# Kernel tuning notes

Measured on AMD Instinct MI355X. Metric: run time of the kernel, lower is better.

Reference implementation:

```python
import jax, jax.numpy as jnp
import numpy as np


def setup_inputs() -> dict:
    key = jax.random.key(0)
    ks = jax.random.split(key, 7)
    B, C, N, F = 4, 8, 2048, 64
    H, O = 64, 64
    s_in = 1.0 / np.sqrt(F)
    s_h = 1.0 / np.sqrt(H)
    return {
        "x": jax.random.normal(ks[0], (B, C, N, F), dtype=jnp.float32),
        "W1": jax.random.uniform(ks[1], (H, F), jnp.float32, -s_in, s_in),
        "b1": jax.random.uniform(ks[2], (H,), jnp.float32, -s_in, s_in),
        "W2": jax.random.uniform(ks[3], (H, F), jnp.float32, -s_in, s_in),
        "b2": jax.random.uniform(ks[4], (H,), jnp.float32, -s_in, s_in),
        "W3": jax.random.uniform(ks[5], (O, F), jnp.float32, -s_in, s_in),
        "b3": jax.random.uniform(ks[6], (O,), jnp.float32, -s_in, s_in),
    }


def reference(x, W1, b1, W2, b2, W3, b3):
    # e1, e2: [B,C,N,H]  (torch Linear: x @ W^T + b)
    e1 = jnp.einsum("bcnf,hf->bcnh", x, W1) + b1
    e2 = jnp.einsum("bcnf,hf->bcnh", x, W2) + b2
    # adjacency via ReLU(e1 @ e2^T): [B,C,N,N]
    adj = jax.nn.relu(jnp.einsum("bcnh,bcmh->bcnm", e1, e2))
    # propagate: [B,C,N,F]
    h = jnp.einsum("bcnm,bcmf->bcnf", adj, x)
    # output projection (linear3): [B,C,N,O]
    return jnp.einsum("bcnf,of->bcno", h, W3) + b3
```

## Files before the change

### kernel.cpp

```cpp
#include <hip/hip_runtime.h>
#include <hip/hip_bf16.h>

#define BCH 32
#define NN  2048
#define DD  64

typedef __attribute__((ext_vector_type(8)))  __bf16 bf16x8;
typedef __attribute__((ext_vector_type(4)))  __bf16 bf16x4;
typedef __attribute__((ext_vector_type(4)))  float  f32x4;
typedef __attribute__((ext_vector_type(16))) float  f32x16;
typedef __attribute__((ext_vector_type(2)))  int    i32x2;
typedef __attribute__((ext_vector_type(4)))  int    i32x4;
typedef __attribute__((ext_vector_type(2)))  unsigned int u32x2;

__device__ inline f32x4 mfma16(bf16x8 a, bf16x8 b, f32x4 c) {
    return __builtin_amdgcn_mfma_f32_16x16x32_bf16(a, b, c, 0, 0, 0);
}
__device__ inline f32x16 mfma32(bf16x8 a, bf16x8 b, f32x16 c) {
    return __builtin_amdgcn_mfma_f32_32x32x16_bf16(a, b, c, 0, 0, 0);
}
__device__ inline void gload16(const void* g, void* l) {
    __builtin_amdgcn_global_load_lds(
        (const __attribute__((address_space(1))) void*)g,
        (__attribute__((address_space(3))) void*)l, 16, 0, 0);
}
__device__ inline void plswap(int& a, int& b) {
    u32x2 r = __builtin_amdgcn_permlane32_swap((unsigned)a, (unsigned)b, false, false);
    a = (int)r[0];
    b = (int)r[1];
}

__global__ __launch_bounds__(256) void prep_kernel(
    const float* __restrict__ x,
    const float* __restrict__ W1, const float* __restrict__ b1,
    const float* __restrict__ W2, const float* __restrict__ b2,
    const float* __restrict__ W3,
    __bf16* __restrict__ e1f, __bf16* __restrict__ e2f, __bf16* __restrict__ vtf)
{
    const int t   = threadIdx.x;
    const int blk = blockIdx.x;
    const int bc  = blk >> 5, st = blk & 31;
    const long grow = (long)bc * NN + st * 64;
    const int w = t >> 6, l = t & 63, lg = l >> 4, li = l & 15;

    bf16x8 a[4][2];
    #pragma unroll
    for (int nb = 0; nb < 4; ++nb)
        #pragma unroll
        for (int kk = 0; kk < 2; ++kk) {
            const float* p = x + (grow + nb * 16 + li) * DD + kk * 32 + lg * 8;
            f32x4 v0 = *(const f32x4*)p, v1 = *(const f32x4*)(p + 4);
            #pragma unroll
            for (int j = 0; j < 4; ++j) {
                a[nb][kk][j]     = (__bf16)v0[j];
                a[nb][kk][4 + j] = (__bf16)v1[j];
            }
        }

    bf16x8 wf1[2], wf2[2], wf3[2];
    #pragma unroll
    for (int kk = 0; kk < 2; ++kk) {
        const float* p1 = W1 + (w * 16 + li) * DD + kk * 32 + lg * 8;
        const float* p2 = W2 + (w * 16 + li) * DD + kk * 32 + lg * 8;
        const float* p3 = W3 + (w * 16 + li) * DD + kk * 32 + lg * 8;
        f32x4 u0 = *(const f32x4*)p1, u1 = *(const f32x4*)(p1 + 4);
        f32x4 v0 = *(const f32x4*)p2, v1 = *(const f32x4*)(p2 + 4);
        f32x4 t0 = *(const f32x4*)p3, t1 = *(const f32x4*)(p3 + 4);
        #pragma unroll
        for (int j = 0; j < 4; ++j) {
            wf1[kk][j] = (__bf16)u0[j]; wf1[kk][4 + j] = (__bf16)u1[j];
            wf2[kk][j] = (__bf16)v0[j]; wf2[kk][4 + j] = (__bf16)v1[j];
            wf3[kk][j] = (__bf16)t0[j]; wf3[kk][4 + j] = (__bf16)t1[j];
        }
    }
    const f32x4 bq1 = *(const f32x4*)(b1 + w * 16 + lg * 4);
    const f32x4 bq2 = *(const f32x4*)(b2 + w * 16 + lg * 4);

    const size_t tbase = (size_t)(bc * 32 + st) * 4096;

    #pragma unroll
    for (int nb = 0; nb < 4; ++nb) {
        f32x4 acc1 = {0.f,0.f,0.f,0.f}, acc2 = {0.f,0.f,0.f,0.f}, acc3 = {0.f,0.f,0.f,0.f};
        #pragma unroll
        for (int kk = 0; kk < 2; ++kk) {
            acc1 = mfma16(wf1[kk], a[nb][kk], acc1);
            acc2 = mfma16(wf2[kk], a[nb][kk], acc2);
            acc3 = mfma16(a[nb][kk], wf3[kk], acc3);
        }
        bf16x4 q1, q2, q3;
        #pragma unroll
        for (int r = 0; r < 4; ++r) {
            q1[r] = (__bf16)(acc1[r] + bq1[r]);
            q2[r] = (__bf16)(acc2[r] + bq2[r]);
            q3[r] = (__bf16)acc3[r];
        }
        *(bf16x4*)&e1f[tbase + (w * 2 + (lg >> 1)) * 512 + (nb * 16 + li) * 8 + (lg & 1) * 4] = q1;
        *(bf16x4*)&e2f[tbase + (w * 2 + (lg >> 1)) * 512 + (nb * 16 + li) * 8 + (lg & 1) * 4] = q2;
        *(bf16x4*)&vtf[tbase + (nb * 2 + (lg >> 1)) * 512 + (w * 16 + li) * 8 + (lg & 1) * 4] = q3;
    }
}

__global__ __launch_bounds__(512, 1) void fused_kernel(
    const __bf16* __restrict__ e1f, const __bf16* __restrict__ e2f,
    const __bf16* __restrict__ vtf, const float* __restrict__ b3,
    float* __restrict__ out)
{
    __shared__ __align__(16) __bf16 tile[2][8192];

    const int t   = threadIdx.x;
    const int bid = blockIdx.x;
    const int j5  = bid & 31;
    const int bc  = (j5 & 7) * 4 + (j5 >> 3);
    const int nt  = bid >> 5;

    const int w = t >> 6, l = t & 63;
    const int wn = w & 3, wm = w >> 2;
    const int l31 = l & 31, hi5 = l >> 5;
    const int nbase = nt * 256 + wn * 64;

    const float bv0 = b3[l31], bv1 = b3[32 + l31];

    bf16x8 e1v[2][4];
    #pragma unroll
    for (int nb = 0; nb < 2; ++nb) {
        const __bf16* p = e1f + ((size_t)bc * 32 + nt * 4 + wn) * 4096 + hi5 * 512 + (nb * 32 + l31) * 8;
        #pragma unroll
        for (int kk = 0; kk < 4; ++kk)
            e1v[nb][kk] = *(const bf16x8*)(p + kk * 1024);
    }

    f32x16 fz;
    #pragma unroll
    for (int i = 0; i < 16; ++i) fz[i] = 0.f;
    f32x16 hacc[2][2];
    #pragma unroll
    for (int nb = 0; nb < 2; ++nb)
        #pragma unroll
        for (int fb = 0; fb < 2; ++fb)
            #pragma unroll
            for (int i = 0; i < 16; ++i) hacc[nb][fb][i] = 0.f;

    const __bf16* E2T = e2f + (size_t)bc * 131072;
    const __bf16* VTT = vtf + (size_t)bc * 131072;

    auto stage = [&](int buf, int kt) {
        gload16(E2T + (size_t)kt * 4096 + t * 8, &tile[buf][w * 512]);
        gload16(VTT + (size_t)kt * 4096 + t * 8, &tile[buf][4096 + w * 512]);
    };

    stage(0, 0);

    for (int kt = 0; kt < 32; ++kt) {
        const int buf = kt & 1;
        if (kt + 1 < 32) {
            stage(buf ^ 1, kt + 1);
            asm volatile("s_waitcnt vmcnt(2)" ::: "memory");
        } else {
            asm volatile("s_waitcnt vmcnt(0)" ::: "memory");
        }
        __builtin_amdgcn_sched_barrier(0);
        __builtin_amdgcn_s_barrier();

        bf16x8 ef[4];
        #pragma unroll
        for (int kk = 0; kk < 4; ++kk)
            ef[kk] = *(const bf16x8*)&tile[buf][kk * 1024 + hi5 * 512 + (wm * 32 + l31) * 8];

        f32x16 sT[2];
        __builtin_amdgcn_s_setprio(1);
        sT[0] = mfma32(ef[0], e1v[0][0], fz);
        sT[1] = mfma32(ef[0], e1v[1][0], fz);
        #pragma unroll
        for (int kk = 1; kk < 4; ++kk) {
            sT[0] = mfma32(ef[kk], e1v[0][kk], sT[0]);
            sT[1] = mfma32(ef[kk], e1v[1][kk], sT[1]);
        }
        __builtin_amdgcn_s_setprio(0);

        i32x2 Q[2][4];
        #pragma unroll
        for (int nb = 0; nb < 2; ++nb)
            #pragma unroll
            for (int g = 0; g < 4; ++g) {
                bf16x4 q0;
                #pragma unroll
                for (int r = 0; r < 4; ++r)
                    q0[r] = (__bf16)fmaxf(sT[nb][4 * g + r], 0.f);
                Q[nb][g] = __builtin_bit_cast(i32x2, q0);
            }

        bf16x8 vf[4];
        #pragma unroll
        for (int kk2 = 0; kk2 < 2; ++kk2) {
            vf[kk2 * 2 + 0] = *(const bf16x8*)&tile[buf][4096 + (wm * 4 + hi5) * 512 + kk2 * 1024 + l31 * 8];
            vf[kk2 * 2 + 1] = *(const bf16x8*)&tile[buf][4096 + (wm * 4 + hi5) * 512 + kk2 * 1024 + 256 + l31 * 8];
        }
        __builtin_amdgcn_s_setprio(1);
        #pragma unroll
        for (int kk2 = 0; kk2 < 2; ++kk2)
            #pragma unroll
            for (int nb = 0; nb < 2; ++nb) {
                int a0 = Q[nb][2 * kk2][0],     a1 = Q[nb][2 * kk2][1];
                int b0 = Q[nb][2 * kk2 + 1][0], b1 = Q[nb][2 * kk2 + 1][1];
                plswap(a0, b0);
                plswap(a1, b1);
                i32x4 pfi = { a0, a1, b0, b1 };
                bf16x8 pf = __builtin_bit_cast(bf16x8, pfi);
                hacc[nb][0] = mfma32(pf, vf[kk2 * 2 + 0], hacc[nb][0]);
                hacc[nb][1] = mfma32(pf, vf[kk2 * 2 + 1], hacc[nb][1]);
            }
        __builtin_amdgcn_s_setprio(0);

        __builtin_amdgcn_s_barrier();
    }

    float* scratch = (float*)&tile[0][0];
    #pragma unroll
    for (int r2 = 0; r2 < 2; ++r2) {
        __syncthreads();
        if ((wn >> 1) == r2 && wm == 1) {
            #pragma unroll
            for (int nb = 0; nb < 2; ++nb)
                #pragma unroll
                for (int q = 0; q < 8; ++q) {
                    f32x4 v;
                    #pragma unroll
                    for (int r = 0; r < 4; ++r) {
                        const int idx = q * 4 + r;
                        v[r] = hacc[nb][idx >> 4][idx & 15];
                    }
                    *(f32x4*)&scratch[(wn & 1) * 4096 + nb * 2048 + q * 256 + l * 4] = v;
                }
        }
        __syncthreads();
        if ((wn >> 1) == r2 && wm == 0) {
            #pragma unroll
            for (int nb = 0; nb < 2; ++nb)
                #pragma unroll
                for (int q = 0; q < 8; ++q) {
                    f32x4 v = *(const f32x4*)&scratch[(wn & 1) * 4096 + nb * 2048 + q * 256 + l * 4];
                    #pragma unroll
                    for (int r = 0; r < 4; ++r) {
                        const int idx = q * 4 + r;
                        hacc[nb][idx >> 4][idx & 15] += v[r];
                    }
                }
            #pragma unroll
            for (int nb = 0; nb < 2; ++nb) {
                const size_t ob = ((size_t)bc * NN + nbase + nb * 32) * DD;
                #pragma unroll
                for (int reg = 0; reg < 16; ++reg) {
                    const int n = (reg & 3) + 8 * (reg >> 2) + 4 * hi5;
                    out[ob + (size_t)n * DD + l31]      = hacc[nb][0][reg] + bv0;
                    out[ob + (size_t)n * DD + 32 + l31] = hacc[nb][1][reg] + bv1;
                }
            }
        }
    }
}

extern "C" void kernel_launch(void* const* d_in, const int* in_sizes, int n_in,
                              void* d_out, int out_size, void* d_ws, size_t ws_size,
                              hipStream_t stream) {
    const float* x  = (const float*)d_in[0];
    const float* W1 = (const float*)d_in[1];
    const float* b1 = (const float*)d_in[2];
    const float* W2 = (const float*)d_in[3];
    const float* b2 = (const float*)d_in[4];
    const float* W3 = (const float*)d_in[5];
    const float* b3 = (const float*)d_in[6];
    float* out = (float*)d_out;

    __bf16* e1f = (__bf16*)d_ws;
    __bf16* e2f = e1f + (size_t)BCH * NN * DD;
    __bf16* vtf = e2f + (size_t)BCH * NN * DD;

    prep_kernel<<<dim3(1024), dim3(256), 0, stream>>>(x, W1, b1, W2, b2, W3, e1f, e2f, vtf);
    fused_kernel<<<dim3(256), dim3(512), 0, stream>>>(e1f, e2f, vtf, b3, out);
}
```

Measured before the change: 59.56 us.

## Fuse projection prep into attention kernel via cooperative grid sync

Merges the separate projection kernel into the main kernel, launched cooperatively with 256 blocks, and uses a grid-wide sync between the projection phase and the adjacency/propagation phase. Each block computes e1 for its own rows directly into shared memory instead of writing it to global memory and reading it back. e2 and the transformed V still go through global memory. The change removes one kernel launch and the e1 global round-trip. In exchange it adds the cost of a grid barrier, redundant W loads per wave, and extra LDS use that may limit occupancy.

```diff
diff --git a/kernel.cpp b/kernel.cpp
--- a/kernel.cpp
+++ b/kernel.cpp
@@ -1,9 +1,12 @@
 #include <hip/hip_runtime.h>
 #include <hip/hip_bf16.h>
+#include <hip/hip_cooperative_groups.h>
 
 #define BCH 32
 #define NN  2048
 #define DD  64
+
+namespace cg = cooperative_groups;
 
 typedef __attribute__((ext_vector_type(8)))  __bf16 bf16x8;
 typedef __attribute__((ext_vector_type(4)))  __bf16 bf16x4;
@@ -30,82 +33,16 @@
     b = (int)r[1];
 }
 
-__global__ __launch_bounds__(256) void prep_kernel(
+__global__ __launch_bounds__(512, 1) void gcn_kernel(
     const float* __restrict__ x,
     const float* __restrict__ W1, const float* __restrict__ b1,
     const float* __restrict__ W2, const float* __restrict__ b2,
-    const float* __restrict__ W3,
-    __bf16* __restrict__ e1f, __bf16* __restrict__ e2f, __bf16* __restrict__ vtf)
-{
-    const int t   = threadIdx.x;
-    const int blk = blockIdx.x;
-    const int bc  = blk >> 5, st = blk & 31;
-    const long grow = (long)bc * NN + st * 64;
-    const int w = t >> 6, l = t & 63, lg = l >> 4, li = l & 15;
-
-    bf16x8 a[4][2];
-    #pragma unroll
-    for (int nb = 0; nb < 4; ++nb)
-        #pragma unroll
-        for (int kk = 0; kk < 2; ++kk) {
-            const float* p = x + (grow + nb * 16 + li) * DD + kk * 32 + lg * 8;
-            f32x4 v0 = *(const f32x4*)p, v1 = *(const f32x4*)(p + 4);
-            #pragma unroll
-            for (int j = 0; j < 4; ++j) {
-                a[nb][kk][j]     = (__bf16)v0[j];
-                a[nb][kk][4 + j] = (__bf16)v1[j];
-            }
-        }
-
-    bf16x8 wf1[2], wf2[2], wf3[2];
-    #pragma unroll
-    for (int kk = 0; kk < 2; ++kk) {
-        const float* p1 = W1 + (w * 16 + li) * DD + kk * 32 + lg * 8;
-        const float* p2 = W2 + (w * 16 + li) * DD + kk * 32 + lg * 8;
-        const float* p3 = W3 + (w * 16 + li) * DD + kk * 32 + lg * 8;
-        f32x4 u0 = *(const f32x4*)p1, u1 = *(const f32x4*)(p1 + 4);
-        f32x4 v0 = *(const f32x4*)p2, v1 = *(const f32x4*)(p2 + 4);
-        f32x4 t0 = *(const f32x4*)p3, t1 = *(const f32x4*)(p3 + 4);
-        #pragma unroll
-        for (int j = 0; j < 4; ++j) {
-            wf1[kk][j] = (__bf16)u0[j]; wf1[kk][4 + j] = (__bf16)u1[j];
-            wf2[kk][j] = (__bf16)v0[j]; wf2[kk][4 + j] = (__bf16)v1[j];
-            wf3[kk][j] = (__bf16)t0[j]; wf3[kk][4 + j] = (__bf16)t1[j];
-        }
-    }
-    const f32x4 bq1 = *(const f32x4*)(b1 + w * 16 + lg * 4);
-    const f32x4 bq2 = *(const f32x4*)(b2 + w * 16 + lg * 4);
-
-    const size_t tbase = (size_t)(bc * 32 + st) * 4096;
-
-    #pragma unroll
-    for (int nb = 0; nb < 4; ++nb) {
-        f32x4 acc1 = {0.f,0.f,0.f,0.f}, acc2 = {0.f,0.f,0.f,0.f}, acc3 = {0.f,0.f,0.f,0.f};
-        #pragma unroll
-        for (int kk = 0; kk < 2; ++kk) {
-            acc1 = mfma16(wf1[kk], a[nb][kk], acc1);
-            acc2 = mfma16(wf2[kk], a[nb][kk], acc2);
-            acc3 = mfma16(a[nb][kk], wf3[kk], acc3);
-        }
-        bf16x4 q1, q2, q3;
-        #pragma unroll
-        for (int r = 0; r < 4; ++r) {
-            q1[r] = (__bf16)(acc1[r] + bq1[r]);
-            q2[r] = (__bf16)(acc2[r] + bq2[r]);
-            q3[r] = (__bf16)acc3[r];
-        }
-        *(bf16x4*)&e1f[tbase + (w * 2 + (lg >> 1)) * 512 + (nb * 16 + li) * 8 + (lg & 1) * 4] = q1;
-        *(bf16x4*)&e2f[tbase + (w * 2 + (lg >> 1)) * 512 + (nb * 16 + li) * 8 + (lg & 1) * 4] = q2;
-        *(bf16x4*)&vtf[tbase + (nb * 2 + (lg >> 1)) * 512 + (w * 16 + li) * 8 + (lg & 1) * 4] = q3;
-    }
-}
-
-__global__ __launch_bounds__(512, 1) void fused_kernel(
-    const __bf16* __restrict__ e1f, const __bf16* __restrict__ e2f,
-    const __bf16* __restrict__ vtf, const float* __restrict__ b3,
+    const float* __restrict__ W3, const float* __restrict__ b3,
+    __bf16* __restrict__ e2f, __bf16* __restrict__ vtf,
     float* __restrict__ out)
 {
     __shared__ __align__(16) __bf16 tile[2][8192];
+    __shared__ __align__(16) __bf16 e1L[8 * 2048];
 
     const int t   = threadIdx.x;
     const int bid = blockIdx.x;
@@ -114,6 +51,73 @@
     const int nt  = bid >> 5;
 
     const int w = t >> 6, l = t & 63;
+    const int lg = l >> 4, li = l & 15;
+
+    {
+        const long growA = (long)bc * NN + nt * 256 + w * 32;
+
+        bf16x8 a[2][2];
+        #pragma unroll
+        for (int nb = 0; nb < 2; ++nb)
+            #pragma unroll
+            for (int kk = 0; kk < 2; ++kk) {
+                const float* p = x + (growA + nb * 16 + li) * DD + kk * 32 + lg * 8;
+                f32x4 v0 = *(const f32x4*)p, v1 = *(const f32x4*)(p + 4);
+                #pragma unroll
+                for (int j = 0; j < 4; ++j) {
+                    a[nb][kk][j]     = (__bf16)v0[j];
+                    a[nb][kk][4 + j] = (__bf16)v1[j];
+                }
+            }
+
+        const size_t tbase = (size_t)(bc * 32 + nt * 4 + (w >> 1)) * 4096;
+
+        #pragma unroll
+        for (int hb = 0; hb < 4; ++hb) {
+            bf16x8 wf1[2], wf2[2], wf3[2];
+            #pragma unroll
+            for (int kk = 0; kk < 2; ++kk) {
+                const float* p1 = W1 + (hb * 16 + li) * DD + kk * 32 + lg * 8;
+                const float* p2 = W2 + (hb * 16 + li) * DD + kk * 32 + lg * 8;
+                const float* p3 = W3 + (hb * 16 + li) * DD + kk * 32 + lg * 8;
+                f32x4 u0 = *(const f32x4*)p1, u1 = *(const f32x4*)(p1 + 4);
+                f32x4 v0 = *(const f32x4*)p2, v1 = *(const f32x4*)(p2 + 4);
+                f32x4 t0 = *(const f32x4*)p3, t1 = *(const f32x4*)(p3 + 4);
+                #pragma unroll
+                for (int j = 0; j < 4; ++j) {
+                    wf1[kk][j] = (__bf16)u0[j]; wf1[kk][4 + j] = (__bf16)u1[j];
+                    wf2[kk][j] = (__bf16)v0[j]; wf2[kk][4 + j] = (__bf16)v1[j];
+                    wf3[kk][j] = (__bf16)t0[j]; wf3[kk][4 + j] = (__bf16)t1[j];
+                }
+            }
+            const f32x4 bq1 = *(const f32x4*)(b1 + hb * 16 + lg * 4);
+            const f32x4 bq2 = *(const f32x4*)(b2 + hb * 16 + lg * 4);
+
+            #pragma unroll
+            for (int nb = 0; nb < 2; ++nb) {
+                f32x4 acc1 = {0.f,0.f,0.f,0.f}, acc2 = {0.f,0.f,0.f,0.f}, acc3 = {0.f,0.f,0.f,0.f};
+                #pragma unroll
+                for (int kk = 0; kk < 2; ++kk) {
+                    acc1 = mfma16(wf1[kk], a[nb][kk], acc1);
+                    acc2 = mfma16(wf2[kk], a[nb][kk], acc2);
+                    acc3 = mfma16(a[nb][kk], wf3[kk], acc3);
+                }
+                bf16x4 q1, q2, q3;
+                #pragma unroll
+                for (int r = 0; r < 4; ++r) {
+                    q1[r] = (__bf16)(acc1[r] + bq1[r]);
+                    q2[r] = (__bf16)(acc2[r] + bq2[r]);
+                    q3[r] = (__bf16)acc3[r];
+                }
+                *(bf16x4*)&e1L[(hb * 2 + (lg >> 1)) * 2048 + (w * 32 + nb * 16 + li) * 8 + (lg & 1) * 4] = q1;
+                *(bf16x4*)&e2f[tbase + (hb * 2 + (lg >> 1)) * 512 + ((w & 1) * 32 + nb * 16 + li) * 8 + (lg & 1) * 4] = q2;
+                *(bf16x4*)&vtf[tbase + ((w & 1) * 4 + nb * 2 + (lg >> 1)) * 512 + (hb * 16 + li) * 8 + (lg & 1) * 4] = q3;
+            }
+        }
+    }
+
+    cg::this_grid().sync();
+
     const int wn = w & 3, wm = w >> 2;
     const int l31 = l & 31, hi5 = l >> 5;
     const int nbase = nt * 256 + wn * 64;
@@ -122,12 +126,10 @@
 
     bf16x8 e1v[2][4];
     #pragma unroll
-    for (int nb = 0; nb < 2; ++nb) {
-        const __bf16* p = e1f + ((size_t)bc * 32 + nt * 4 + wn) * 4096 + hi5 * 512 + (nb * 32 + l31) * 8;
+    for (int nb = 0; nb < 2; ++nb)
         #pragma unroll
         for (int kk = 0; kk < 4; ++kk)
-            e1v[nb][kk] = *(const bf16x8*)(p + kk * 1024);
-    }
+            e1v[nb][kk] = *(const bf16x8*)&e1L[(kk * 2 + hi5) * 2048 + (wn * 64 + nb * 32 + l31) * 8];
 
     f32x16 fz;
     #pragma unroll
@@ -271,10 +273,11 @@
     const float* b3 = (const float*)d_in[6];
     float* out = (float*)d_out;
 
-    __bf16* e1f = (__bf16*)d_ws;
-    __bf16* e2f = e1f + (size_t)BCH * NN * DD;
+    __bf16* e2f = (__bf16*)d_ws;
     __bf16* vtf = e2f + (size_t)BCH * NN * DD;
 
-    prep_kernel<<<dim3(1024), dim3(256), 0, stream>>>(x, W1, b1, W2, b2, W3, e1f, e2f, vtf);
-    fused_kernel<<<dim3(256), dim3(512), 0, stream>>>(e1f, e2f, vtf, b3, out);
-}
+    void* args[] = { (void*)&x, (void*)&W1, (void*)&b1, (void*)&W2, (void*)&b2,
+                     (void*)&W3, (void*)&b3, (void*)&e2f, (void*)&vtf, (void*)&out };
+    hipLaunchCooperativeKernel((const void*)gcn_kernel, dim3(256), dim3(512),
+                               args, 0, stream);
+}
```

After: 87.91 us. 47.6% more time.
